# Kernel optimization log

Hardware: AMD Instinct MI355X
Metric: run time of the kernel (lower is better)

The kernel has to match this reference:

```python
import jax, jax.numpy as jnp
import numpy as np

EPS = 1e-5
KQ_DIM = 512

def layer_norm(x, g, b):
    mu = jnp.mean(x, axis=-1, keepdims=True)
    var = jnp.mean((x - mu) ** 2, axis=-1, keepdims=True)
    return (x - mu) * jax.lax.rsqrt(var + EPS) * g + b

def setup_inputs() -> dict:
    key = jax.random.key(0)
    ks = jax.random.split(key, 8)
    B, Sq, Skv = 8, 2048, 2048
    vk_i_dim, q_i_dim, kq_dim = 512, 512, KQ_DIM
    vals = jax.random.normal(ks[0], (B, Skv, vk_i_dim), jnp.float32)
    keys = jax.random.normal(ks[1], (B, Skv, vk_i_dim), jnp.float32)
    ques = jax.random.normal(ks[2], (B, Sq, q_i_dim), jnp.float32)
    # causal: mask out strictly-upper triangle (future keys)
    causal_mask = jnp.triu(jnp.ones((Sq, Skv), jnp.bool_), k=1)
    key_mask = jnp.zeros((B, Skv), jnp.bool_)
    s = 1.0 / np.sqrt(vk_i_dim)
    Wv = jax.random.normal(ks[3], (vk_i_dim, q_i_dim), jnp.float32) * s
    Wk = jax.random.normal(ks[4], (vk_i_dim, kq_dim), jnp.float32) * s
    Wq = jax.random.normal(ks[5], (q_i_dim, kq_dim), jnp.float32) * (1.0 / np.sqrt(q_i_dim))
    return {
        "vals": vals, "keys": keys, "ques": ques,
        "causal_mask": causal_mask, "key_mask": key_mask,
        "Wv": Wv, "Wk": Wk, "Wq": Wq,
        "ln_k_g": jnp.ones((kq_dim,), jnp.float32), "ln_k_b": jnp.zeros((kq_dim,), jnp.float32),
        "ln_q_g": jnp.ones((kq_dim,), jnp.float32), "ln_q_b": jnp.zeros((kq_dim,), jnp.float32),
        "ln_o_g": jnp.ones((q_i_dim,), jnp.float32), "ln_o_b": jnp.zeros((q_i_dim,), jnp.float32),
    }

def reference(vals, keys, ques, causal_mask, key_mask, Wv, Wk, Wq,
              ln_k_g, ln_k_b, ln_q_g, ln_q_b, ln_o_g, ln_o_b):
    v = vals @ Wv                                   # [B, Skv, q_i_dim]
    k = layer_norm(keys @ Wk, ln_k_g, ln_k_b)       # [B, Skv, kq_dim]
    q = layer_norm(ques @ Wq, ln_q_g, ln_q_b)       # [B, Sq, kq_dim]
    a = jnp.einsum('bqd,bkd->bqk', q, k) / jnp.sqrt(jnp.asarray(KQ_DIM, q.dtype))
    neg_inf = jnp.asarray(-jnp.inf, a.dtype)
    a = jnp.where(causal_mask[None, :, :], neg_inf, a)
    a = jnp.where(key_mask[:, None, :], neg_inf, a)
    p = jax.nn.softmax(a, axis=-1)
    o = jnp.einsum('bqk,bkd->bqd', p, v)            # dropout = identity (eval)
    return layer_norm(o + ques, ln_o_g, ln_o_b)
```

## Files before the change

### kernel.cpp

```cpp
#include <hip/hip_runtime.h>
#include <cstdint>

typedef short bf8 __attribute__((ext_vector_type(8)));
typedef float f4 __attribute__((ext_vector_type(4)));

#define SEQ 2048
#define DIM 512
#define NMAT (512*512)
#define SCQ 0.04419417382415922f
#define LOG2E 1.4426950408889634f

__device__ inline unsigned short f2bf(float f){
    unsigned int u = __builtin_bit_cast(unsigned int, f);
    u = (u + 0x7FFFu + ((u >> 16) & 1u)) >> 16;
    return (unsigned short)u;
}

__device__ __forceinline__ float exp2fast(float x){
    return __builtin_amdgcn_exp2f(x);
}

__device__ __forceinline__ void glds16(const unsigned short* gsrc, const unsigned short* ldst){
    __builtin_amdgcn_global_load_lds(
        (const __attribute__((address_space(1))) unsigned int*)gsrc,
        (__attribute__((address_space(3))) unsigned int*)ldst, 16, 0, 0);
}

template<int CTRL>
__device__ __forceinline__ float dppadd(float x){
    const int t = __builtin_amdgcn_update_dpp(0, __builtin_bit_cast(int, x), CTRL, 0xF, 0xF, true);
    return x + __builtin_bit_cast(float, t);
}
template<int CTRL>
__device__ __forceinline__ float dppmax(float x){
    const int t = __builtin_amdgcn_update_dpp(0, __builtin_bit_cast(int, x), CTRL, 0xF, 0xF, true);
    return fmaxf(x, __builtin_bit_cast(float, t));
}

__global__ void prep_w(const float* __restrict__ Wv, const float* __restrict__ Wk,
                       const float* __restrict__ Wq, unsigned short* __restrict__ Wt)
{
    __shared__ float t_lds[64][65];
    const int m = blockIdx.y;
    const float* W = (m == 0) ? Wv : ((m == 1) ? Wk : Wq);
    const int bn = (blockIdx.x & 7) * 64;
    const int bk = (blockIdx.x >> 3) * 64;
    const int tr = threadIdx.x >> 6;
    const int tc = threadIdx.x & 63;
    #pragma unroll
    for (int i = 0; i < 16; ++i){
        const int k = tr + 4 * i;
        t_lds[k][tc] = W[(size_t)(bk + k) * 512 + bn + tc];
    }
    __syncthreads();
    #pragma unroll
    for (int i = 0; i < 16; ++i){
        const int n = tr + 4 * i;
        Wt[(size_t)m * NMAT + (size_t)(bn + n) * 512 + bk + tc] = f2bf(t_lds[tc][n]);
    }
}

__global__ __launch_bounds__(512, 4) void gemm3(
    const float* __restrict__ vals, const float* __restrict__ keys, const float* __restrict__ ques,
    const unsigned short* __restrict__ Wt,
    const float* __restrict__ kg, const float* __restrict__ kbe,
    const float* __restrict__ qg, const float* __restrict__ qbe,
    unsigned short* __restrict__ vt, unsigned short* __restrict__ kbuf, unsigned short* __restrict__ qbuf)
{
    __shared__ unsigned short a_lds[64 * DIM];
    float* red1    = (float*)a_lds;
    float* red2    = red1 + 512;
    float* stat_mu = red2 + 512;
    float* stat_rs = stat_mu + 64;

    const int tid = threadIdx.x;
    const int wv  = tid >> 6;
    const int l   = tid & 63;
    const int g   = l >> 4;
    const int lr  = l & 15;
    const int gid = blockIdx.x;
    const int m   = gid >> 8;
    const int r0  = (gid & 255) * 64;
    const float* X = (m == 0) ? vals : ((m == 1) ? keys : ques);
    const unsigned short* W = Wt + m * NMAT;

    {
        const int row = tid >> 3;
        const int cb  = (tid & 7) * 4;
        const float* xr = X + (size_t)(r0 + row) * DIM;
        #pragma unroll
        for (int i = 0; i < 16; ++i){
            const int col = cb + i * 32;
            const float4 v = *reinterpret_cast<const float4*>(xr + col);
            ushort4 h;
            h.x = f2bf(v.x); h.y = f2bf(v.y); h.z = f2bf(v.z); h.w = f2bf(v.w);
            const int byte = ((row * DIM + col) * 2) ^ ((row & 7) << 4);
            *reinterpret_cast<ushort4*>(reinterpret_cast<char*>(a_lds) + byte) = h;
        }
    }
    __syncthreads();

    f4 acc[4][4];
    #pragma unroll
    for (int i = 0; i < 4; ++i)
        #pragma unroll
        for (int j = 0; j < 4; ++j)
            acc[i][j] = (f4){0.f, 0.f, 0.f, 0.f};

    const int nb = wv * 64;
    #pragma unroll 4
    for (int ks = 0; ks < 16; ++ks){
        const int kof = ks * 32 + g * 8;
        bf8 af[4], bfr[4];
        #pragma unroll
        for (int rt = 0; rt < 4; ++rt){
            const int row = 16 * rt + lr;
            const int byte = ((row * DIM + kof) * 2) ^ ((row & 7) << 4);
            af[rt] = *reinterpret_cast<const bf8*>(reinterpret_cast<const char*>(a_lds) + byte);
        }
        #pragma unroll
        for (int ct = 0; ct < 4; ++ct)
            bfr[ct] = *reinterpret_cast<const bf8*>(W + (size_t)(nb + 16 * ct + lr) * DIM + kof);
        #pragma unroll
        for (int rt = 0; rt < 4; ++rt)
            #pragma unroll
            for (int ct = 0; ct < 4; ++ct)
                acc[rt][ct] = __builtin_amdgcn_mfma_f32_16x16x32_bf16(af[rt], bfr[ct], acc[rt][ct], 0, 0, 0);
    }

    if (m == 0){
        __syncthreads();
        #pragma unroll
        for (int rt = 0; rt < 4; ++rt)
            #pragma unroll
            for (int r = 0; r < 4; ++r){
                const int row = 16 * rt + g * 4 + r;
                #pragma unroll
                for (int ct = 0; ct < 4; ++ct){
                    const int d = nb + 16 * ct + lr;
                    const int byte = (d * 128 + row * 2) ^ ((d & 7) << 4);
                    *reinterpret_cast<unsigned short*>(reinterpret_cast<char*>(a_lds) + byte) = f2bf(acc[rt][ct][r]);
                }
            }
        __syncthreads();
        const int bb = r0 >> 11;
        const int s0 = r0 & 2047;
        #pragma unroll
        for (int pq = 0; pq < 4; ++pq){
            const int d  = pq * 128 + (tid >> 2);
            const int sc = (tid & 3) * 16;
            const int base = d * 128 + sc * 2;
            const int sw = (d & 7) << 4;
            const bf8 x0 = *reinterpret_cast<const bf8*>(reinterpret_cast<const char*>(a_lds) + (base ^ sw));
            const bf8 x1 = *reinterpret_cast<const bf8*>(reinterpret_cast<const char*>(a_lds) + ((base + 16) ^ sw));
            unsigned short* dst = vt + (size_t)(bb * 512 + d) * SEQ + s0 + sc;
            *reinterpret_cast<bf8*>(dst)     = x0;
            *reinterpret_cast<bf8*>(dst + 8) = x1;
        }
        return;
    }

    const float* gamma = (m == 1) ? kg  : qg;
    const float* beta  = (m == 1) ? kbe : qbe;
    const float scale  = (m == 1) ? 1.0f : SCQ * LOG2E;
    unsigned short* outp = (m == 1) ? kbuf : qbuf;

    __syncthreads();
    #pragma unroll
    for (int rt = 0; rt < 4; ++rt){
        #pragma unroll
        for (int r = 0; r < 4; ++r){
            float s1 = 0.f, s2 = 0.f;
            #pragma unroll
            for (int ct = 0; ct < 4; ++ct){ const float v = acc[rt][ct][r]; s1 += v; s2 += v * v; }
            s1 = dppadd<0xB1>(s1); s1 = dppadd<0x4E>(s1); s1 = dppadd<0x141>(s1); s1 = dppadd<0x140>(s1);
            s2 = dppadd<0xB1>(s2); s2 = dppadd<0x4E>(s2); s2 = dppadd<0x141>(s2); s2 = dppadd<0x140>(s2);
            if (lr == 0){
                const int row = 16 * rt + g * 4 + r;
                red1[row * 8 + wv] = s1;
                red2[row * 8 + wv] = s2;
            }
        }
    }
    __syncthreads();
    if (tid < 64){
        float S1 = 0.f, S2 = 0.f;
        #pragma unroll
        for (int w = 0; w < 8; ++w){ S1 += red1[tid * 8 + w]; S2 += red2[tid * 8 + w]; }
        const float mu = S1 * (1.0f / 512.0f);
        const float var = S2 * (1.0f / 512.0f) - mu * mu;
        stat_mu[tid] = mu;
        stat_rs[tid] = rsqrtf(var + 1e-5f);
    }
    __syncthreads();
    #pragma unroll
    for (int rt = 0; rt < 4; ++rt){
        #pragma unroll
        for (int r = 0; r < 4; ++r){
            const int row = 16 * rt + g * 4 + r;
            const float mu = stat_mu[row];
            const float rs = stat_rs[row];
            #pragma unroll
            for (int ct = 0; ct < 4; ++ct){
                const int d = nb + 16 * ct + lr;
                const float v = ((acc[rt][ct][r] - mu) * rs * gamma[d] + beta[d]) * scale;
                outp[(size_t)(r0 + row) * DIM + d] = f2bf(v);
            }
        }
    }
}

__global__ __launch_bounds__(512, 2) void attn(
    const unsigned short* __restrict__ qb, const unsigned short* __restrict__ kb,
    const unsigned short* __restrict__ vt, const float* __restrict__ qin,
    const float* __restrict__ g_o, const float* __restrict__ b_o,
    float* __restrict__ outp)
{
    __shared__ unsigned short k_lds[4 * 32 * DIM];
    __shared__ float s_lds[64][68];
    __shared__ unsigned short p_lds[64 * 64];
    __shared__ float l_lds[64], fac_lds[64];
    float* red1    = &s_lds[0][0];
    float* red2    = red1 + 512;
    float* stat_mu = red2 + 512;
    float* stat_rs = stat_mu + 64;

    const int tid = threadIdx.x;
    const int wv  = tid >> 6;
    const int l   = tid & 63;
    const int g   = l >> 4;
    const int lr  = l & 15;
    const int b   = blockIdx.x & 7;
    const int p   = blockIdx.x >> 3;
    const int q0a = 32 * p;
    const int q0b = 32 * (63 - p);
    const int n2  = (65 - p) >> 1;
    const int jL  = p >> 1;

    const int ct  = wv & 1;
    const int rt_ = wv >> 1;

    bf8 qf[16];
    {
        const int row = 16 * rt_ + lr;
        const int qglob = (row < 32) ? (q0a + row) : (q0b + row - 32);
        const unsigned short* qr = qb + (size_t)(b * SEQ + qglob) * DIM + g * 8;
        #pragma unroll
        for (int ks = 0; ks < 16; ++ks)
            qf[ks] = *reinterpret_cast<const bf8*>(qr + ks * 32);
    }

    auto kglds = [&](int t){
        const int bo = (t & 3) * (32 * DIM);
        #pragma unroll
        for (int i = 0; i < 4; ++i){
            const int row = 4 * wv + i;
            glds16(kb + (size_t)(b * SEQ + t * 32 + row) * DIM + ((l * 8) ^ ((row & 7) * 8)),
                   k_lds + bo + row * DIM);
        }
    };

    kglds(0);
    kglds(1);

    float m_reg = -__builtin_inff();
    float l_reg = 0.0f;

    f4 acc[4][4];
    #pragma unroll
    for (int rt = 0; rt < 4; ++rt)
        #pragma unroll
        for (int cv = 0; cv < 4; ++cv)
            acc[rt][cv] = (f4){0.f, 0.f, 0.f, 0.f};
    bf8 vst[8];

    asm volatile("s_waitcnt vmcnt(0)" ::: "memory");
    __builtin_amdgcn_s_barrier();
    __builtin_amdgcn_sched_barrier(0);

    auto do_pv = [&](int jp){
        const bool frozen = (jp > jL);
        __builtin_amdgcn_s_setprio(1);
        #pragma unroll
        for (int rt = 0; rt < 4; ++rt){
            if (rt < 2 && frozen) continue;
            float f[4];
            #pragma unroll
            for (int r = 0; r < 4; ++r) f[r] = fac_lds[16 * rt + 4 * g + r];
            #pragma unroll
            for (int cv = 0; cv < 4; ++cv)
                #pragma unroll
                for (int r = 0; r < 4; ++r)
                    acc[rt][cv][r] *= f[r];
            const int prow = 16 * rt + lr;
            const int sw = (prow & 7) << 4;
            const bf8 pa0 = *reinterpret_cast<const bf8*>(
                reinterpret_cast<const char*>(p_lds) + prow * 128 + ((g * 16) ^ sw));
            const bf8 pa1 = *reinterpret_cast<const bf8*>(
                reinterpret_cast<const char*>(p_lds) + prow * 128 + ((64 + g * 16) ^ sw));
            #pragma unroll
            for (int cv = 0; cv < 4; ++cv){
                acc[rt][cv] = __builtin_amdgcn_mfma_f32_16x16x32_bf16(pa0, vst[2 * cv],     acc[rt][cv], 0, 0, 0);
                acc[rt][cv] = __builtin_amdgcn_mfma_f32_16x16x32_bf16(pa1, vst[2 * cv + 1], acc[rt][cv], 0, 0, 0);
            }
        }
        __builtin_amdgcn_s_setprio(0);
    };

    for (int j = 0; j < n2; ++j){
        const int k0 = 64 * j;
        const int tp = 2 * j + 2;
        if (tp     < 2 * n2) kglds(tp);
        if (tp + 1 < 2 * n2) kglds(tp + 1);

        if (j > 0) do_pv(j - 1);

        #pragma unroll
        for (int cv = 0; cv < 4; ++cv)
            #pragma unroll
            for (int ks = 0; ks < 2; ++ks)
                vst[2 * cv + ks] = *reinterpret_cast<const bf8*>(
                    vt + (size_t)(b * DIM + 64 * wv + 16 * cv + lr) * SEQ + k0 + 32 * ks + g * 8);

        if (rt_ >= 2 || j <= jL){
            const int krow  = 16 * ct + lr;
            const int rbase = krow * 1024;
            const int rx    = (krow & 7) << 4;
            __builtin_amdgcn_s_setprio(1);
            #pragma unroll
            for (int h = 0; h < 2; ++h){
                const char* kbuf = reinterpret_cast<const char*>(k_lds) + ((2 * j + h) & 3) * 32768;
                f4 sa[4];
                sa[0] = (f4){0.f,0.f,0.f,0.f}; sa[1] = (f4){0.f,0.f,0.f,0.f};
                sa[2] = (f4){0.f,0.f,0.f,0.f}; sa[3] = (f4){0.f,0.f,0.f,0.f};
                #pragma unroll
                for (int ks = 0; ks < 16; ++ks){
                    const bf8 bk = *reinterpret_cast<const bf8*>(
                        kbuf + rbase + ((ks * 64 + g * 16) ^ rx));
                    sa[ks & 3] = __builtin_amdgcn_mfma_f32_16x16x32_bf16(qf[ks], bk, sa[ks & 3], 0, 0, 0);
                }
                const f4 s = (sa[0] + sa[1]) + (sa[2] + sa[3]);
                const int srow = 16 * rt_ + 4 * g;
                #pragma unroll
                for (int r = 0; r < 4; ++r)
                    s_lds[srow + r][32 * h + 16 * ct + lr] = s[r];
            }
            __builtin_amdgcn_s_setprio(0);
        }
        asm volatile("s_waitcnt lgkmcnt(0)" ::: "memory");
        __builtin_amdgcn_s_barrier();
        __builtin_amdgcn_sched_barrier(0);

        {
            const int row = tid >> 3;
            const int cp  = tid & 7;
            if (row >= 32 || j <= jL){
                const float4 x0 = *reinterpret_cast<const float4*>(&s_lds[row][8 * cp]);
                const float4 x1 = *reinterpret_cast<const float4*>(&s_lds[row][8 * cp + 4]);
                float av[8] = {x0.x, x0.y, x0.z, x0.w, x1.x, x1.y, x1.z, x1.w};
                const int qrow = (row < 32) ? (q0a + row) : (q0b + row - 32);
                const int kc = k0 + 8 * cp;
                #pragma unroll
                for (int jj = 0; jj < 8; ++jj)
                    if (kc + jj > qrow) av[jj] = -1e30f;
                float pm = fmaxf(fmaxf(fmaxf(av[0], av[1]), fmaxf(av[2], av[3])),
                                 fmaxf(fmaxf(av[4], av[5]), fmaxf(av[6], av[7])));
                pm = dppmax<0xB1>(pm); pm = dppmax<0x4E>(pm); pm = dppmax<0x141>(pm);
                const float mo = m_reg;
                const float mn = fmaxf(mo, pm);
                float e[8];
                #pragma unroll
                for (int jj = 0; jj < 8; ++jj) e[jj] = exp2fast(av[jj] - mn);
                float ts = ((e[0] + e[1]) + (e[2] + e[3])) + ((e[4] + e[5]) + (e[6] + e[7]));
                ts = dppadd<0xB1>(ts); ts = dppadd<0x4E>(ts); ts = dppadd<0x141>(ts);
                const float fc = exp2fast(mo - mn);
                m_reg = mn;
                l_reg = l_reg * fc + ts;
                if (cp == 0) fac_lds[row] = fc;
                uint4 pk;
                pk.x = (unsigned int)f2bf(e[0]) | ((unsigned int)f2bf(e[1]) << 16);
                pk.y = (unsigned int)f2bf(e[2]) | ((unsigned int)f2bf(e[3]) << 16);
                pk.z = (unsigned int)f2bf(e[4]) | ((unsigned int)f2bf(e[5]) << 16);
                pk.w = (unsigned int)f2bf(e[6]) | ((unsigned int)f2bf(e[7]) << 16);
                *reinterpret_cast<uint4*>(reinterpret_cast<char*>(p_lds) +
                    row * 128 + ((cp * 16) ^ ((row & 7) << 4))) = pk;
            }
        }
        asm volatile("s_waitcnt vmcnt(8)" ::: "memory");
        asm volatile("s_waitcnt lgkmcnt(0)" ::: "memory");
        __builtin_amdgcn_s_barrier();
        __builtin_amdgcn_sched_barrier(0);
    }

    if ((tid & 7) == 0) l_lds[tid >> 3] = l_reg;

    asm volatile("s_waitcnt vmcnt(0)" ::: "memory");
    do_pv(n2 - 1);
    __syncthreads();

    float li[4][4];
    #pragma unroll
    for (int rt = 0; rt < 4; ++rt)
        #pragma unroll
        for (int r = 0; r < 4; ++r)
            li[rt][r] = 1.0f / l_lds[16 * rt + 4 * g + r];
    #pragma unroll
    for (int rt = 0; rt < 4; ++rt){
        #pragma unroll
        for (int cv = 0; cv < 4; ++cv){
            #pragma unroll
            for (int r = 0; r < 4; ++r){
                const int row = 16 * rt + 4 * g + r;
                const int qglob = (row < 32) ? (q0a + row) : (q0b + row - 32);
                const int d = 64 * wv + 16 * cv + lr;
                acc[rt][cv][r] = acc[rt][cv][r] * li[rt][r]
                               + qin[(size_t)(b * SEQ + qglob) * DIM + d];
            }
        }
    }
    __syncthreads();
    #pragma unroll
    for (int rt = 0; rt < 4; ++rt){
        #pragma unroll
        for (int r = 0; r < 4; ++r){
            float s1 = 0.f, s2 = 0.f;
            #pragma unroll
            for (int cv = 0; cv < 4; ++cv){ const float v = acc[rt][cv][r]; s1 += v; s2 += v * v; }
            s1 = dppadd<0xB1>(s1); s1 = dppadd<0x4E>(s1); s1 = dppadd<0x141>(s1); s1 = dppadd<0x140>(s1);
            s2 = dppadd<0xB1>(s2); s2 = dppadd<0x4E>(s2); s2 = dppadd<0x141>(s2); s2 = dppadd<0x140>(s2);
            if (lr == 0){
                const int row = 16 * rt + 4 * g + r;
                red1[row * 8 + wv] = s1;
                red2[row * 8 + wv] = s2;
            }
        }
    }
    __syncthreads();
    if (tid < 64){
        float S1 = 0.f, S2 = 0.f;
        #pragma unroll
        for (int w = 0; w < 8; ++w){ S1 += red1[tid * 8 + w]; S2 += red2[tid * 8 + w]; }
        const float mu = S1 * (1.0f / 512.0f);
        const float var = S2 * (1.0f / 512.0f) - mu * mu;
        stat_mu[tid] = mu;
        stat_rs[tid] = rsqrtf(var + 1e-5f);
    }
    __syncthreads();
    #pragma unroll
    for (int rt = 0; rt < 4; ++rt){
        #pragma unroll
        for (int r = 0; r < 4; ++r){
            const int row = 16 * rt + 4 * g + r;
            const int qglob = (row < 32) ? (q0a + row) : (q0b + row - 32);
            const float mu = stat_mu[row];
            const float rs = stat_rs[row];
            #pragma unroll
            for (int cv = 0; cv < 4; ++cv){
                const int d = 64 * wv + 16 * cv + lr;
                outp[(size_t)(b * SEQ + qglob) * DIM + d] =
                    (acc[rt][cv][r] - mu) * rs * g_o[d] + b_o[d];
            }
        }
    }
}

extern "C" void kernel_launch(void* const* d_in, const int* in_sizes, int n_in,
                              void* d_out, int out_size, void* d_ws, size_t ws_size,
                              hipStream_t stream)
{
    (void)in_sizes; (void)n_in; (void)out_size; (void)ws_size;
    const float* vals = (const float*)d_in[0];
    const float* keys = (const float*)d_in[1];
    const float* ques = (const float*)d_in[2];
    const float* Wv   = (const float*)d_in[5];
    const float* Wk   = (const float*)d_in[6];
    const float* Wq   = (const float*)d_in[7];
    const float* ln_k_g = (const float*)d_in[8];
    const float* ln_k_b = (const float*)d_in[9];
    const float* ln_q_g = (const float*)d_in[10];
    const float* ln_q_b = (const float*)d_in[11];
    const float* ln_o_g = (const float*)d_in[12];
    const float* ln_o_b = (const float*)d_in[13];
    float* outp = (float*)d_out;

    char* ws = (char*)d_ws;
    unsigned short* qbuf = (unsigned short*)(ws);
    unsigned short* kbuf = (unsigned short*)(ws + (size_t)16 * 1024 * 1024);
    unsigned short* vt   = (unsigned short*)(ws + (size_t)32 * 1024 * 1024);
    unsigned short* Wt   = (unsigned short*)(ws + (size_t)48 * 1024 * 1024);

    prep_w<<<dim3(64, 3), 256, 0, stream>>>(Wv, Wk, Wq, Wt);

    gemm3<<<768, 512, 0, stream>>>(vals, keys, ques, Wt,
                                   ln_k_g, ln_k_b, ln_q_g, ln_q_b,
                                   vt, kbuf, qbuf);

    attn<<<256, 512, 0, stream>>>(qbuf, kbuf, vt, ques, ln_o_g, ln_o_b, outp);
}
```

Before: 185.0 us.

## Software-pipeline attention loop with 32-key tiles, triple-buffered K, double-buffered S/P

Restructures the attention main loop from 64-key steps with two barriers into 32-key steps with one barrier per iteration. QK^T for tile j, softmax for tile j-1 and PV for tile j-2 run in the same iteration, using double-buffered score, probability and scale-factor buffers in shared memory. K is triple-buffered in LDS instead of quad-buffered. This is meant to overlap softmax work with MFMA work and halve the barrier count per key. In exchange it doubles the iteration count, which adds per-step overhead and gives smaller MFMA batches per step.

```diff
diff --git a/kernel.cpp b/kernel.cpp
--- a/kernel.cpp
+++ b/kernel.cpp
@@ -216,11 +216,12 @@
     const float* __restrict__ g_o, const float* __restrict__ b_o,
     float* __restrict__ outp)
 {
-    __shared__ unsigned short k_lds[4 * 32 * DIM];
-    __shared__ float s_lds[64][68];
-    __shared__ unsigned short p_lds[64 * 64];
-    __shared__ float l_lds[64], fac_lds[64];
-    float* red1    = &s_lds[0][0];
+    __shared__ unsigned short k_lds[3 * 32 * DIM];
+    __shared__ float s_dbuf[2][64][36];
+    __shared__ unsigned short p_dbuf[2][64 * 40];
+    __shared__ float fac_dbuf[2][64];
+    __shared__ float l_lds[64];
+    float* red1    = &s_dbuf[0][0][0];
     float* red2    = red1 + 512;
     float* stat_mu = red2 + 512;
     float* stat_rs = stat_mu + 64;
@@ -234,8 +235,7 @@
     const int p   = blockIdx.x >> 3;
     const int q0a = 32 * p;
     const int q0b = 32 * (63 - p);
-    const int n2  = (65 - p) >> 1;
-    const int jL  = p >> 1;
+    const int n   = 64 - p;
 
     const int ct  = wv & 1;
     const int rt_ = wv >> 1;
@@ -250,8 +250,8 @@
             qf[ks] = *reinterpret_cast<const bf8*>(qr + ks * 32);
     }
 
-    auto kglds = [&](int t){
-        const int bo = (t & 3) * (32 * DIM);
+    auto kglds = [&](int slot, int t){
+        const int bo = slot * (32 * DIM);
         #pragma unroll
         for (int i = 0; i < 4; ++i){
             const int row = 4 * wv + i;
@@ -260,8 +260,8 @@
         }
     };
 
-    kglds(0);
-    kglds(1);
+    kglds(0, 0);
+    kglds(1, 1);
 
     float m_reg = -__builtin_inff();
     float l_reg = 0.0f;
@@ -272,130 +272,133 @@
         #pragma unroll
         for (int cv = 0; cv < 4; ++cv)
             acc[rt][cv] = (f4){0.f, 0.f, 0.f, 0.f};
-    bf8 vst[8];
+    bf8 vst[4];
 
     asm volatile("s_waitcnt vmcnt(0)" ::: "memory");
     __builtin_amdgcn_s_barrier();
     __builtin_amdgcn_sched_barrier(0);
 
     auto do_pv = [&](int jp){
-        const bool frozen = (jp > jL);
+        const bool frozen = (jp > p);
+        const char* pb  = reinterpret_cast<const char*>(p_dbuf[jp & 1]);
+        const float* fc = fac_dbuf[jp & 1];
         __builtin_amdgcn_s_setprio(1);
         #pragma unroll
         for (int rt = 0; rt < 4; ++rt){
             if (rt < 2 && frozen) continue;
             float f[4];
             #pragma unroll
-            for (int r = 0; r < 4; ++r) f[r] = fac_lds[16 * rt + 4 * g + r];
+            for (int r = 0; r < 4; ++r) f[r] = fc[16 * rt + 4 * g + r];
             #pragma unroll
             for (int cv = 0; cv < 4; ++cv)
                 #pragma unroll
                 for (int r = 0; r < 4; ++r)
                     acc[rt][cv][r] *= f[r];
-            const int prow = 16 * rt + lr;
-            const int sw = (prow & 7) << 4;
-            const bf8 pa0 = *reinterpret_cast<const bf8*>(
-                reinterpret_cast<const char*>(p_lds) + prow * 128 + ((g * 16) ^ sw));
-            const bf8 pa1 = *reinterpret_cast<const bf8*>(
-                reinterpret_cast<const char*>(p_lds) + prow * 128 + ((64 + g * 16) ^ sw));
-            #pragma unroll
-            for (int cv = 0; cv < 4; ++cv){
-                acc[rt][cv] = __builtin_amdgcn_mfma_f32_16x16x32_bf16(pa0, vst[2 * cv],     acc[rt][cv], 0, 0, 0);
-                acc[rt][cv] = __builtin_amdgcn_mfma_f32_16x16x32_bf16(pa1, vst[2 * cv + 1], acc[rt][cv], 0, 0, 0);
-            }
+            const bf8 pa = *reinterpret_cast<const bf8*>(pb + (16 * rt + lr) * 80 + g * 16);
+            #pragma unroll
+            for (int cv = 0; cv < 4; ++cv)
+                acc[rt][cv] = __builtin_amdgcn_mfma_f32_16x16x32_bf16(pa, vst[cv], acc[rt][cv], 0, 0, 0);
         }
         __builtin_amdgcn_s_setprio(0);
     };
 
-    for (int j = 0; j < n2; ++j){
-        const int k0 = 64 * j;
-        const int tp = 2 * j + 2;
-        if (tp     < 2 * n2) kglds(tp);
-        if (tp + 1 < 2 * n2) kglds(tp + 1);
-
-        if (j > 0) do_pv(j - 1);
-
-        #pragma unroll
-        for (int cv = 0; cv < 4; ++cv)
-            #pragma unroll
-            for (int ks = 0; ks < 2; ++ks)
-                vst[2 * cv + ks] = *reinterpret_cast<const bf8*>(
-                    vt + (size_t)(b * DIM + 64 * wv + 16 * cv + lr) * SEQ + k0 + 32 * ks + g * 8);
-
-        if (rt_ >= 2 || j <= jL){
+    auto do_sm = [&](int tj){
+        const int row = tid >> 3;
+        const int cp  = tid & 7;
+        if (row >= 32 || tj <= p){
+            const float4 x0 = *reinterpret_cast<const float4*>(&s_dbuf[tj & 1][row][4 * cp]);
+            float av[4] = {x0.x, x0.y, x0.z, x0.w};
+            const int qrow = (row < 32) ? (q0a + row) : (q0b + row - 32);
+            const int kc = 32 * tj + 4 * cp;
+            #pragma unroll
+            for (int jj = 0; jj < 4; ++jj)
+                if (kc + jj > qrow) av[jj] = -1e30f;
+            float pm = fmaxf(fmaxf(av[0], av[1]), fmaxf(av[2], av[3]));
+            pm = dppmax<0xB1>(pm); pm = dppmax<0x4E>(pm); pm = dppmax<0x141>(pm);
+            const float mo = m_reg;
+            const float mn = fmaxf(mo, pm);
+            float e[4];
+            #pragma unroll
+            for (int jj = 0; jj < 4; ++jj) e[jj] = exp2fast(av[jj] - mn);
+            float ts = (e[0] + e[1]) + (e[2] + e[3]);
+            ts = dppadd<0xB1>(ts); ts = dppadd<0x4E>(ts); ts = dppadd<0x141>(ts);
+            const float fc = exp2fast(mo - mn);
+            m_reg = mn;
+            l_reg = l_reg * fc + ts;
+            if (cp == 0) fac_dbuf[tj & 1][row] = fc;
+            uint2 pk;
+            pk.x = (unsigned int)f2bf(e[0]) | ((unsigned int)f2bf(e[1]) << 16);
+            pk.y = (unsigned int)f2bf(e[2]) | ((unsigned int)f2bf(e[3]) << 16);
+            *reinterpret_cast<uint2*>(reinterpret_cast<char*>(p_dbuf[tj & 1]) +
+                row * 80 + cp * 8) = pk;
+        }
+    };
+
+    for (int j = 0; j < n; ++j){
+        kglds((j + 2) % 3, j + 2 < n ? j + 2 : 0);
+
+        asm volatile("s_waitcnt vmcnt(4)" ::: "memory");
+        __builtin_amdgcn_sched_barrier(0);
+
+        if (j >= 2) do_pv(j - 2);
+
+        if (j >= 1){
+            const int k0 = 32 * (j - 1);
+            #pragma unroll
+            for (int cv = 0; cv < 4; ++cv)
+                vst[cv] = *reinterpret_cast<const bf8*>(
+                    vt + (size_t)(b * DIM + 64 * wv + 16 * cv + lr) * SEQ + k0 + g * 8);
+        }
+
+        if (rt_ >= 2 || j <= p){
             const int krow  = 16 * ct + lr;
             const int rbase = krow * 1024;
             const int rx    = (krow & 7) << 4;
+            const char* kbuf = reinterpret_cast<const char*>(k_lds) + (j % 3) * 32768;
             __builtin_amdgcn_s_setprio(1);
-            #pragma unroll
-            for (int h = 0; h < 2; ++h){
-                const char* kbuf = reinterpret_cast<const char*>(k_lds) + ((2 * j + h) & 3) * 32768;
-                f4 sa[4];
-                sa[0] = (f4){0.f,0.f,0.f,0.f}; sa[1] = (f4){0.f,0.f,0.f,0.f};
-                sa[2] = (f4){0.f,0.f,0.f,0.f}; sa[3] = (f4){0.f,0.f,0.f,0.f};
-                #pragma unroll
-                for (int ks = 0; ks < 16; ++ks){
-                    const bf8 bk = *reinterpret_cast<const bf8*>(
-                        kbuf + rbase + ((ks * 64 + g * 16) ^ rx));
-                    sa[ks & 3] = __builtin_amdgcn_mfma_f32_16x16x32_bf16(qf[ks], bk, sa[ks & 3], 0, 0, 0);
-                }
-                const f4 s = (sa[0] + sa[1]) + (sa[2] + sa[3]);
-                const int srow = 16 * rt_ + 4 * g;
-                #pragma unroll
-                for (int r = 0; r < 4; ++r)
-                    s_lds[srow + r][32 * h + 16 * ct + lr] = s[r];
-            }
+            f4 sa[4];
+            sa[0] = (f4){0.f,0.f,0.f,0.f}; sa[1] = (f4){0.f,0.f,0.f,0.f};
+            sa[2] = (f4){0.f,0.f,0.f,0.f}; sa[3] = (f4){0.f,0.f,0.f,0.f};
+            #pragma unroll
+            for (int ks = 0; ks < 16; ++ks){
+                const bf8 bk = *reinterpret_cast<const bf8*>(
+                    kbuf + rbase + ((ks * 64 + g * 16) ^ rx));
+                sa[ks & 3] = __builtin_amdgcn_mfma_f32_16x16x32_bf16(qf[ks], bk, sa[ks & 3], 0, 0, 0);
+            }
+            const f4 s = (sa[0] + sa[1]) + (sa[2] + sa[3]);
+            const int srow = 16 * rt_ + 4 * g;
+            #pragma unroll
+            for (int r = 0; r < 4; ++r)
+                s_dbuf[j & 1][srow + r][16 * ct + lr] = s[r];
             __builtin_amdgcn_s_setprio(0);
         }
+
+        if (j >= 1) do_sm(j - 1);
+
         asm volatile("s_waitcnt lgkmcnt(0)" ::: "memory");
         __builtin_amdgcn_s_barrier();
         __builtin_amdgcn_sched_barrier(0);
-
-        {
-            const int row = tid >> 3;
-            const int cp  = tid & 7;
-            if (row >= 32 || j <= jL){
-                const float4 x0 = *reinterpret_cast<const float4*>(&s_lds[row][8 * cp]);
-                const float4 x1 = *reinterpret_cast<const float4*>(&s_lds[row][8 * cp + 4]);
-                float av[8] = {x0.x, x0.y, x0.z, x0.w, x1.x, x1.y, x1.z, x1.w};
-                const int qrow = (row < 32) ? (q0a + row) : (q0b + row - 32);
-                const int kc = k0 + 8 * cp;
-                #pragma unroll
-                for (int jj = 0; jj < 8; ++jj)
-                    if (kc + jj > qrow) av[jj] = -1e30f;
-                float pm = fmaxf(fmaxf(fmaxf(av[0], av[1]), fmaxf(av[2], av[3])),
-                                 fmaxf(fmaxf(av[4], av[5]), fmaxf(av[6], av[7])));
-                pm = dppmax<0xB1>(pm); pm = dppmax<0x4E>(pm); pm = dppmax<0x141>(pm);
-                const float mo = m_reg;
-                const float mn = fmaxf(mo, pm);
-                float e[8];
-                #pragma unroll
-                for (int jj = 0; jj < 8; ++jj) e[jj] = exp2fast(av[jj] - mn);
-                float ts = ((e[0] + e[1]) + (e[2] + e[3])) + ((e[4] + e[5]) + (e[6] + e[7]));
-                ts = dppadd<0xB1>(ts); ts = dppadd<0x4E>(ts); ts = dppadd<0x141>(ts);
-                const float fc = exp2fast(mo - mn);
-                m_reg = mn;
-                l_reg = l_reg * fc + ts;
-                if (cp == 0) fac_lds[row] = fc;
-                uint4 pk;
-                pk.x = (unsigned int)f2bf(e[0]) | ((unsigned int)f2bf(e[1]) << 16);
-                pk.y = (unsigned int)f2bf(e[2]) | ((unsigned int)f2bf(e[3]) << 16);
-                pk.z = (unsigned int)f2bf(e[4]) | ((unsigned int)f2bf(e[5]) << 16);
-                pk.w = (unsigned int)f2bf(e[6]) | ((unsigned int)f2bf(e[7]) << 16);
-                *reinterpret_cast<uint4*>(reinterpret_cast<char*>(p_lds) +
-                    row * 128 + ((cp * 16) ^ ((row & 7) << 4))) = pk;
-            }
-        }
-        asm volatile("s_waitcnt vmcnt(8)" ::: "memory");
-        asm volatile("s_waitcnt lgkmcnt(0)" ::: "memory");
-        __builtin_amdgcn_s_barrier();
-        __builtin_amdgcn_sched_barrier(0);
-    }
+    }
+
+    asm volatile("s_waitcnt vmcnt(0)" ::: "memory");
+    __builtin_amdgcn_sched_barrier(0);
+    do_pv(n - 2);
+    {
+        const int k0 = 32 * (n - 1);
+        #pragma unroll
+        for (int cv = 0; cv < 4; ++cv)
+            vst[cv] = *reinterpret_cast<const bf8*>(
+                vt + (size_t)(b * DIM + 64 * wv + 16 * cv + lr) * SEQ + k0 + g * 8);
+    }
+    do_sm(n - 1);
+    asm volatile("s_waitcnt lgkmcnt(0)" ::: "memory");
+    __builtin_amdgcn_s_barrier();
+    __builtin_amdgcn_sched_barrier(0);
+    asm volatile("s_waitcnt vmcnt(0)" ::: "memory");
+    __builtin_amdgcn_sched_barrier(0);
+    do_pv(n - 1);
 
     if ((tid & 7) == 0) l_lds[tid >> 3] = l_reg;
-
-    asm volatile("s_waitcnt vmcnt(0)" ::: "memory");
-    do_pv(n2 - 1);
     __syncthreads();
 
     float li[4][4];
```

Result: no change. 185.7 us (+0.4%).
